# Performance work log

Measured on AMD Instinct MI355X. Metric: run time of the kernel, lower is better.

The kernel has to match this reference:

```python
import jax, jax.numpy as jnp
import numpy as np

B, C, T, E = 8, 64, 128, 256
TYPE_NUM, NF = 40, 128
KS = (5, 4, 3)
NEG = -1e10


def setup_inputs() -> dict:
    key = jax.random.key(0)
    ks = jax.random.split(key, 10)
    s = 0.02
    return {
        "query": jax.random.normal(ks[0], (C, E), jnp.float32),
        "context": jax.random.normal(ks[1], (B, T, E), jnp.float32),
        "mask": jax.random.randint(ks[2], (B, T), 0, 2, jnp.int32),
        "W_hidden": jax.random.normal(ks[3], (4 * E, 4 * E), jnp.float32) * s,
        "b_hidden": jnp.zeros((4 * E,), jnp.float32),
        "W_v": jax.random.normal(ks[4], (1, 4 * E), jnp.float32) * s,
        "b_v": jnp.zeros((1,), jnp.float32),
        "W_lin": jax.random.normal(ks[5], (E, 4 * E), jnp.float32) * s,
        "b_lin": jnp.zeros((E,), jnp.float32),
        "conv_w0": jax.random.normal(ks[6], (NF, E, KS[0]), jnp.float32) * s,
        "conv_b0": jnp.zeros((NF,), jnp.float32),
        "conv_w1": jax.random.normal(ks[7], (NF, E, KS[1]), jnp.float32) * s,
        "conv_b1": jnp.zeros((NF,), jnp.float32),
        "conv_w2": jax.random.normal(ks[8], (NF, E, KS[2]), jnp.float32) * s,
        "conv_b2": jnp.zeros((NF,), jnp.float32),
        "W_cnn": jax.random.normal(ks[9], (TYPE_NUM, NF * 3), jnp.float32) * s,
        "b_cnn": jnp.zeros((TYPE_NUM,), jnp.float32),
    }


def _pair_feat(a, b):
    # [.., e] x2 -> [.., 4e]: [a, b, |a-b|, a*b]
    return jnp.concatenate([a, b, jnp.abs(a - b), a * b], axis=-1)


def _conv1d(x, w, b):
    # x: [b, e, c], w: [f, e, k] (torch Conv1d layout) -> [b, f, c-k+1]
    y = jax.lax.conv_general_dilated(
        x, w, window_strides=(1,), padding="VALID",
        dimension_numbers=("NCH", "OIH", "NCH"))
    return y + b[None, :, None]


def reference(query, context, mask, W_hidden, b_hidden, W_v, b_v,
              W_lin, b_lin, conv_w0, conv_b0, conv_w1, conv_b1,
              conv_w2, conv_b2, W_cnn, b_cnn):
    b, t, e = context.shape
    c = query.shape[0]
    q_ = jnp.broadcast_to(query[None, :, None, :], (b, c, t, e))
    ctx_ = jnp.broadcast_to(context[:, None, :, :], (b, c, t, e))
    feat = _pair_feat(q_, ctx_)                                 # [b,c,t,4e]
    h = jnp.tanh(feat @ W_hidden.T + b_hidden)                  # [b,c,t,4e]
    scores = (h @ W_v.T + b_v)[..., 0]                          # [b,c,t]
    scores = jnp.where((mask < 1)[:, None, :], NEG, scores)
    attn = jax.nn.softmax(scores, axis=-1)                      # [b,c,t]
    g = jnp.einsum("bct,bte->bce", attn, context)               # [b,c,e]
    q2 = jnp.broadcast_to(query[None], (b, c, e))
    h2 = jnp.tanh(_pair_feat(q2, g) @ W_hidden.T + b_hidden)    # [b,c,4e]
    x = h2 @ W_lin.T + b_lin                                    # [b,c,e]
    xT = jnp.transpose(x, (0, 2, 1))                            # [b,e,c]
    pooled = []
    for w, bb in ((conv_w0, conv_b0), (conv_w1, conv_b1), (conv_w2, conv_b2)):
        y = jax.nn.relu(_conv1d(xT, w, bb))                     # [b,f,c-k+1]
        pooled.append(jnp.max(y, axis=2))                       # [b,f]
    cnn = jnp.concatenate(pooled, axis=1)                       # [b,3f]
    return cnn @ W_cnn.T + b_cnn                                # [b,type_num]
```

## Files before the change

kernel.cpp:

```cpp
#include <hip/hip_runtime.h>
#include <math.h>


typedef __bf16 bf16x8 __attribute__((ext_vector_type(8)));
typedef float  f32x4  __attribute__((ext_vector_type(4)));

__device__ __forceinline__ float ftanh(float v) {
    float t = __expf(2.f * v);
    return 1.f - 2.f * __builtin_amdgcn_rcpf(t + 1.f);
}

__device__ __forceinline__ void gld_lds16(const __bf16* g, __bf16* l) {
    __builtin_amdgcn_global_load_lds(
        (const __attribute__((address_space(1))) void*)g,
        (__attribute__((address_space(3))) void*)l, 16, 0, 0);
}

__global__ __launch_bounds__(256) void gemm_tn_kernel(
    const float* __restrict__ A, int lda,
    const float* __restrict__ B, int ldb,
    const float* __restrict__ bias,
    float* __restrict__ C, int ldc, int K)
{
    __shared__ float As[16][68];
    __shared__ float Bs[16][68];
    const int tid = threadIdx.x;
    const int m0 = blockIdx.y * 64, n0 = blockIdx.x * 64;
    const int tm = tid >> 4, tn = tid & 15;
    const int lr = tid >> 2;
    const int lc = (tid & 3) * 4;

    float acc[4][4];
#pragma unroll
    for (int i = 0; i < 4; ++i)
#pragma unroll
        for (int j = 0; j < 4; ++j) acc[i][j] = 0.f;

    for (int k0 = 0; k0 < K; k0 += 16) {
        float4 av = *reinterpret_cast<const float4*>(A + (size_t)(m0 + lr) * lda + k0 + lc);
        float4 bv = *reinterpret_cast<const float4*>(B + (size_t)(n0 + lr) * ldb + k0 + lc);
        As[lc + 0][lr] = av.x; As[lc + 1][lr] = av.y; As[lc + 2][lr] = av.z; As[lc + 3][lr] = av.w;
        Bs[lc + 0][lr] = bv.x; Bs[lc + 1][lr] = bv.y; Bs[lc + 2][lr] = bv.z; Bs[lc + 3][lr] = bv.w;
        __syncthreads();
#pragma unroll
        for (int kk = 0; kk < 16; ++kk) {
            float4 a = *reinterpret_cast<const float4*>(&As[kk][tm * 4]);
            float4 b = *reinterpret_cast<const float4*>(&Bs[kk][tn * 4]);
            float ar[4] = {a.x, a.y, a.z, a.w};
            float br[4] = {b.x, b.y, b.z, b.w};
#pragma unroll
            for (int i = 0; i < 4; ++i)
#pragma unroll
                for (int j = 0; j < 4; ++j) acc[i][j] += ar[i] * br[j];
        }
        __syncthreads();
    }

#pragma unroll
    for (int i = 0; i < 4; ++i) {
        int m = m0 + tm * 4 + i;
        float vals[4];
#pragma unroll
        for (int j = 0; j < 4; ++j) {
            int n = n0 + tn * 4 + j;
            vals[j] = acc[i][j] + (bias ? bias[n] : 0.f);
        }
        float4 o; o.x = vals[0]; o.y = vals[1]; o.z = vals[2]; o.w = vals[3];
        *reinterpret_cast<float4*>(C + (size_t)m * ldc + n0 + tn * 4) = o;
    }
}

__global__ void cvt_kernel(const float* __restrict__ Wh, const float* __restrict__ Wl,
                           const float* __restrict__ ctx,
                           const float* __restrict__ cw0, const float* __restrict__ cw1,
                           const float* __restrict__ cw2,
                           __bf16* __restrict__ Whbf, __bf16* __restrict__ Whbf_t,
                           __bf16* __restrict__ Wlbf, __bf16* __restrict__ ctxbf,
                           float* __restrict__ wt0, float* __restrict__ wt1,
                           float* __restrict__ wt2, float* __restrict__ gsc,
                           float* __restrict__ cnn)
{
    int idx = blockIdx.x * 256 + threadIdx.x;
    if (idx < 131072) {
        const float* s = Wh + (size_t)idx * 8;
        float4 f0 = *reinterpret_cast<const float4*>(s);
        float4 f1 = *reinterpret_cast<const float4*>(s + 4);
        bf16x8 u;
        u[0] = (__bf16)f0.x; u[1] = (__bf16)f0.y; u[2] = (__bf16)f0.z; u[3] = (__bf16)f0.w;
        u[4] = (__bf16)f1.x; u[5] = (__bf16)f1.y; u[6] = (__bf16)f1.z; u[7] = (__bf16)f1.w;
        *reinterpret_cast<bf16x8*>(Whbf + (size_t)idx * 8) = u;
        return;
    }
    if (idx < 196608) {
        int di = idx - 131072;
        int ng = di >> 13, kc = (di >> 10) & 7;
        int row = (di >> 3) & 127, kgp = di & 7;
        int kg = kgp ^ (row & 7);
        const float* s = Wh + (size_t)(ng * 128 + row) * 1024 + 512 + kc * 64 + kg * 8;
        float4 f0 = *reinterpret_cast<const float4*>(s);
        float4 f1 = *reinterpret_cast<const float4*>(s + 4);
        bf16x8 u;
        u[0] = (__bf16)f0.x; u[1] = (__bf16)f0.y; u[2] = (__bf16)f0.z; u[3] = (__bf16)f0.w;
        u[4] = (__bf16)f1.x; u[5] = (__bf16)f1.y; u[6] = (__bf16)f1.z; u[7] = (__bf16)f1.w;
        *reinterpret_cast<bf16x8*>(Whbf_t + (size_t)di * 8) = u;
        return;
    }
    if (idx < 229376) {
        int di = idx - 196608;
        const float* s = Wl + (size_t)di * 8;
        float4 f0 = *reinterpret_cast<const float4*>(s);
        float4 f1 = *reinterpret_cast<const float4*>(s + 4);
        bf16x8 u;
        u[0] = (__bf16)f0.x; u[1] = (__bf16)f0.y; u[2] = (__bf16)f0.z; u[3] = (__bf16)f0.w;
        u[4] = (__bf16)f1.x; u[5] = (__bf16)f1.y; u[6] = (__bf16)f1.z; u[7] = (__bf16)f1.w;
        *reinterpret_cast<bf16x8*>(Wlbf + (size_t)di * 8) = u;
        return;
    }
    if (idx < 262144) {
        int di = idx - 229376;
        const float* s = ctx + (size_t)di * 8;
        float4 f0 = *reinterpret_cast<const float4*>(s);
        float4 f1 = *reinterpret_cast<const float4*>(s + 4);
        bf16x8 u;
        u[0] = (__bf16)f0.x; u[1] = (__bf16)f0.y; u[2] = (__bf16)f0.z; u[3] = (__bf16)f0.w;
        u[4] = (__bf16)f1.x; u[5] = (__bf16)f1.y; u[6] = (__bf16)f1.z; u[7] = (__bf16)f1.w;
        *reinterpret_cast<bf16x8*>(ctxbf + (size_t)di * 8) = u;
        return;
    }
    if (idx < 425984) {
        int j = idx - 262144; int f = j & 127, rest = j >> 7;
        int i = rest % 5, e = rest / 5;
        wt0[j] = cw0[(size_t)(f * 256 + e) * 5 + i]; return;
    }
    if (idx < 557056) {
        int j = idx - 425984; int f = j & 127, rest = j >> 7;
        int i = rest & 3, e = rest >> 2;
        wt1[j] = cw1[(size_t)(f * 256 + e) * 4 + i]; return;
    }
    if (idx < 655360) {
        int j = idx - 557056; int f = j & 127, rest = j >> 7;
        int i = rest % 3, e = rest / 3;
        wt2[j] = cw2[(size_t)(f * 256 + e) * 3 + i]; return;
    }
    if (idx < 671744) {
        int di = idx - 655360;
        reinterpret_cast<float4*>(gsc)[di] = (float4){0.f, 0.f, 0.f, 0.f};
        return;
    }
    if (idx < 674816) cnn[idx - 671744] = 0.f;
}

__global__ __launch_bounds__(512, 4) void attn_mfma_kernel(
    const float* __restrict__ q,
    const float* __restrict__ ctx,
    const __bf16* __restrict__ Whbf_t,
    const float* __restrict__ Wv,
    const float* __restrict__ Apre,
    const float* __restrict__ Bpre,
    float* __restrict__ gsc)
{
    __shared__ __bf16 Us[256 * 64];
    __shared__ __bf16 Ws[128 * 64];
    __shared__ float qc[512];
    __shared__ float sc[256];

    const int tid = threadIdx.x;
    const int cpair = blockIdx.x >> 3, ng = blockIdx.x & 7;
    const int b = cpair >> 5, c0 = (cpair & 31) * 2;
    const int wave = tid >> 6, lane = tid & 63;
    const int w1 = wave & 1, w0 = wave >> 1;
    const int m0 = w0 * 64;
    const int l15 = lane & 15, quad = lane >> 4;
    const int swz = l15 & 7;
    const int kg = tid & 7;

    qc[tid] = q[(size_t)(c0 + (tid >> 8)) * 256 + (tid & 255)];
    if (tid < 256) sc[tid] = 0.f;
    __syncthreads();

    f32x4 acc[4][4];
#pragma unroll
    for (int mi = 0; mi < 4; ++mi)
#pragma unroll
        for (int ni = 0; ni < 4; ++ni) acc[mi][ni] = (f32x4){0.f, 0.f, 0.f, 0.f};

    for (int kc = 0; kc < 8; ++kc) {
        const bool isabs = (kc < 4);
        const int e0 = (kc & 3) * 64;
        const int eb = e0 + kg * 8;
        float qA[8], qB[8];
#pragma unroll
        for (int i = 0; i < 8; ++i) { qA[i] = qc[eb + i]; qB[i] = qc[256 + eb + i]; }
        bf16x8 u0[2], u1[2];
#pragma unroll
        for (int it = 0; it < 2; ++it) {
            const int trow = it * 64 + (tid >> 3);
            const float* cp = ctx + (size_t)(b * 128 + trow) * 256 + eb;
            float4 cl0 = *reinterpret_cast<const float4*>(cp);
            float4 cl1 = *reinterpret_cast<const float4*>(cp + 4);
            float cv[8] = {cl0.x, cl0.y, cl0.z, cl0.w, cl1.x, cl1.y, cl1.z, cl1.w};
#pragma unroll
            for (int i = 0; i < 8; ++i) {
                u0[it][i] = (__bf16)(isabs ? fabsf(qA[i] - cv[i]) : qA[i] * cv[i]);
                u1[it][i] = (__bf16)(isabs ? fabsf(qB[i] - cv[i]) : qB[i] * cv[i]);
            }
        }
        __syncthreads();
        const __bf16* wtile = Whbf_t + (size_t)(ng * 8 + kc) * 8192;
#pragma unroll
        for (int it = 0; it < 2; ++it) {
            int gidx = wave * 128 + it * 64;
            gld_lds16(wtile + (size_t)(gidx + lane) * 8, &Ws[gidx * 8]);
        }
#pragma unroll
        for (int it = 0; it < 2; ++it) {
            const int trow = it * 64 + (tid >> 3);
            const int off = (kg ^ (trow & 7)) * 8;
            *reinterpret_cast<bf16x8*>(&Us[trow * 64 + off]) = u0[it];
            *reinterpret_cast<bf16x8*>(&Us[(trow + 128) * 64 + off]) = u1[it];
        }
        __syncthreads();
#pragma unroll
        for (int ks = 0; ks < 2; ++ks) {
            const int c8 = (((ks * 4 + quad) ^ swz)) * 8;
            bf16x8 a[4], bfr[4];
#pragma unroll
            for (int mi = 0; mi < 4; ++mi)
                a[mi] = *reinterpret_cast<const bf16x8*>(
                    &Us[(m0 + mi * 16 + l15) * 64 + c8]);
#pragma unroll
            for (int ni = 0; ni < 4; ++ni)
                bfr[ni] = *reinterpret_cast<const bf16x8*>(
                    &Ws[(w1 * 64 + ni * 16 + l15) * 64 + c8]);
#pragma unroll
            for (int mi = 0; mi < 4; ++mi)
#pragma unroll
                for (int ni = 0; ni < 4; ++ni)
                    acc[mi][ni] = __builtin_amdgcn_mfma_f32_16x16x32_bf16(
                        a[mi], bfr[ni], acc[mi][ni], 0, 0, 0);
        }
    }

    const int jcol = ng * 128 + w1 * 64 + l15;
    const int c = c0 + (w0 >> 1);
    float av[4], wv[4];
#pragma unroll
    for (int ni = 0; ni < 4; ++ni) {
        av[ni] = Apre[(size_t)c * 1024 + jcol + ni * 16];
        wv[ni] = Wv[jcol + ni * 16];
    }
#pragma unroll
    for (int mi = 0; mi < 4; ++mi) {
        const int tb = (w0 & 1) * 64 + mi * 16 + quad * 4;
        float p[4];
#pragma unroll
        for (int r = 0; r < 4; ++r) {
            const float* bp = Bpre + (size_t)(b * 128 + tb + r) * 1024 + jcol;
            float s = 0.f;
#pragma unroll
            for (int ni = 0; ni < 4; ++ni)
                s += ftanh(acc[mi][ni][r] + av[ni] + bp[ni * 16]) * wv[ni];
            p[r] = s;
        }
#pragma unroll
        for (int off = 1; off < 16; off <<= 1)
#pragma unroll
            for (int r = 0; r < 4; ++r) p[r] += __shfl_xor(p[r], off, 16);
        if (l15 == 0) {
#pragma unroll
            for (int r = 0; r < 4; ++r)
                atomicAdd(&sc[(w0 >> 1) * 128 + tb + r], p[r]);
        }
    }
    __syncthreads();

    if (tid < 256) atomicAdd(&gsc[(size_t)(b * 64 + c0) * 128 + tid], sc[tid]);
}

__global__ __launch_bounds__(256) void attn_tail_kernel(
    const float* __restrict__ ctx, const int* __restrict__ mask,
    const float* __restrict__ bv, const float* __restrict__ gsc,
    const float* __restrict__ q, __bf16* __restrict__ feat2)
{
    __shared__ float sc[128];
    __shared__ float red;
    const int tid = threadIdx.x;
    const int bc = blockIdx.x, b = bc >> 6, c = bc & 63;

    if (tid < 128) {
        float s = gsc[(size_t)bc * 128 + tid] + bv[0];
        if (mask[b * 128 + tid] < 1) s = -1e10f;
        sc[tid] = s;
    }
    __syncthreads();
    if (tid < 64) {
        float m = fmaxf(sc[tid], sc[tid + 64]);
        for (int off = 32; off; off >>= 1) m = fmaxf(m, __shfl_xor(m, off, 64));
        if (tid == 0) red = m;
    }
    __syncthreads();
    const float mx = red;
    if (tid < 128) sc[tid] = __expf(sc[tid] - mx);
    __syncthreads();
    if (tid < 64) {
        float s = sc[tid] + sc[tid + 64];
        for (int off = 32; off; off >>= 1) s += __shfl_xor(s, off, 64);
        if (tid == 0) red = s;
    }
    __syncthreads();
    const float inv = 1.f / red;

    float gv = 0.f;
    for (int t = 0; t < 128; ++t) gv += sc[t] * ctx[(size_t)(b * 128 + t) * 256 + tid];
    gv *= inv;
    const float qv = q[(size_t)c * 256 + tid];
    __bf16* o = feat2 + (size_t)bc * 768 + tid;
    o[0]   = (__bf16)gv;
    o[256] = (__bf16)fabsf(qv - gv);
    o[512] = (__bf16)(qv * gv);
}

template <int ACT, int OUTBF, int BMODE>
__global__ __launch_bounds__(256) void mfma_gemm_kernel(
    const __bf16* __restrict__ A, int lda,
    const __bf16* __restrict__ B, int ldb,
    const float* __restrict__ bias, void* __restrict__ Cout,
    int K, int ldc)
{
    __shared__ __bf16 As[64 * 72];
    __shared__ __bf16 Bs[64 * 72];
    const int tid = threadIdx.x;
    const int wave = tid >> 6, lane = tid & 63;
    const int w0 = wave >> 1, w1 = wave & 1;
    const int l15 = lane & 15, quad = lane >> 4;
    const int m0 = blockIdx.y * 64, n0 = blockIdx.x * 64;

    f32x4 acc[2][2];
#pragma unroll
    for (int mi = 0; mi < 2; ++mi)
#pragma unroll
        for (int ni = 0; ni < 2; ++ni) acc[mi][ni] = (f32x4){0.f, 0.f, 0.f, 0.f};

    for (int k0 = 0; k0 < K; k0 += 64) {
        __syncthreads();
#pragma unroll
        for (int it = 0; it < 2; ++it) {
            int idx = tid + it * 256;
            int row = idx >> 3, kgi = idx & 7;
            int4 va = *reinterpret_cast<const int4*>(A + (size_t)(m0 + row) * lda + k0 + kgi * 8);
            *reinterpret_cast<int4*>(&As[row * 72 + kgi * 8]) = va;
            int4 vb = *reinterpret_cast<const int4*>(B + (size_t)(n0 + row) * ldb + k0 + kgi * 8);
            *reinterpret_cast<int4*>(&Bs[row * 72 + kgi * 8]) = vb;
        }
        __syncthreads();
#pragma unroll
        for (int ks = 0; ks < 2; ++ks) {
            bf16x8 a[2], bb[2];
#pragma unroll
            for (int mi = 0; mi < 2; ++mi)
                a[mi] = *reinterpret_cast<const bf16x8*>(
                    &As[(w0 * 32 + mi * 16 + l15) * 72 + ks * 32 + quad * 8]);
#pragma unroll
            for (int ni = 0; ni < 2; ++ni)
                bb[ni] = *reinterpret_cast<const bf16x8*>(
                    &Bs[(w1 * 32 + ni * 16 + l15) * 72 + ks * 32 + quad * 8]);
#pragma unroll
            for (int mi = 0; mi < 2; ++mi)
#pragma unroll
                for (int ni = 0; ni < 2; ++ni)
                    acc[mi][ni] = __builtin_amdgcn_mfma_f32_16x16x32_bf16(
                        a[mi], bb[ni], acc[mi][ni], 0, 0, 0);
        }
    }

#pragma unroll
    for (int mi = 0; mi < 2; ++mi)
#pragma unroll
        for (int ni = 0; ni < 2; ++ni) {
            int col = n0 + w1 * 32 + ni * 16 + l15;
#pragma unroll
            for (int r = 0; r < 4; ++r) {
                int row = m0 + w0 * 32 + mi * 16 + quad * 4 + r;
                float bsv = (BMODE == 0) ? bias[col]
                          : (BMODE == 1) ? bias[(row & 63) * 1024 + col] : 0.f;
                float v = acc[mi][ni][r] + bsv;
                if (ACT) v = ftanh(v);
                if (OUTBF) ((__bf16*)Cout)[(size_t)row * ldc + col] = (__bf16)v;
                else       ((float*)Cout)[(size_t)row * ldc + col] = v;
            }
        }
}

template <int KW>
__device__ __forceinline__ void conv_body(
    const float* __restrict__ x, const float* __restrict__ wt,
    float* __restrict__ part, int b, int chunk, int bi_part, int pbase, float* xs)
{
    const int tid = threadIdx.x;
    const int f = tid & 127, esub = tid >> 7;
    const int e0 = chunk * 64;

#pragma unroll
    for (int it = 0; it < 16; ++it) {
        int idx = tid + it * 256;
        int e = idx & 63, p = idx >> 6;
        xs[e * 72 + p] = x[(size_t)(b * 64 + p) * 256 + e0 + e];
    }
    __syncthreads();

    float acc[32];
#pragma unroll
    for (int p = 0; p < 32; ++p) acc[p] = 0.f;

    for (int ei = 0; ei < 32; ++ei) {
        const int eL = esub * 32 + ei;
        float wreg[KW];
#pragma unroll
        for (int i = 0; i < KW; ++i)
            wreg[i] = wt[(size_t)((e0 + eL) * KW + i) * 128 + f];
        float xv[36];
#pragma unroll
        for (int k4 = 0; k4 < 9; ++k4) {
            float4 v = *reinterpret_cast<const float4*>(&xs[eL * 72 + pbase + k4 * 4]);
            xv[k4 * 4 + 0] = v.x; xv[k4 * 4 + 1] = v.y;
            xv[k4 * 4 + 2] = v.z; xv[k4 * 4 + 3] = v.w;
        }
#pragma unroll
        for (int i = 0; i < KW; ++i)
#pragma unroll
            for (int p = 0; p < 32; ++p)
                acc[p] = fmaf(wreg[i], xv[p + i], acc[p]);
    }

    float* op = part + ((size_t)(bi_part * 2 + esub)) * 8192 + f;
#pragma unroll
    for (int p = 0; p < 32; ++p) op[(pbase + p) * 128] = acc[p];
}

__global__ __launch_bounds__(256) void conv_partial_kernel(
    const float* __restrict__ x,
    const float* __restrict__ wt0, const float* __restrict__ wt1,
    const float* __restrict__ wt2, float* __restrict__ part)
{
    __shared__ float xs[64 * 72];
    const int bi = blockIdx.x;
    const int kw = bi >> 6, b = (bi >> 3) & 7, chunk = (bi >> 1) & 3;
    const int pbase = (bi & 1) * 32;
    const int bi_part = kw * 32 + b * 4 + chunk;
    if (kw == 0)      conv_body<5>(x, wt0, part, b, chunk, bi_part, pbase, xs);
    else if (kw == 1) conv_body<4>(x, wt1, part, b, chunk, bi_part, pbase, xs);
    else              conv_body<3>(x, wt2, part, b, chunk, bi_part, pbase, xs);
}

__global__ __launch_bounds__(128) void reduce_pool_kernel(
    const float* __restrict__ part,
    const float* __restrict__ b0, const float* __restrict__ b1,
    const float* __restrict__ b2, float* __restrict__ cnn)
{
    const int bi = blockIdx.x;
    const int kw = bi >> 6, b = (bi >> 3) & 7, pc = bi & 7;
    const int f = threadIdx.x;
    const int KW = 5 - kw, P = 64 - KW + 1;
    const float bias = (kw == 0 ? b0 : kw == 1 ? b1 : b2)[f];
    float mx = 0.f;
#pragma unroll
    for (int pl = 0; pl < 8; ++pl) {
        int p = pc * 8 + pl;
        if (p < P) {
            float s = 0.f;
#pragma unroll
            for (int c4 = 0; c4 < 4; ++c4)
#pragma unroll
                for (int es = 0; es < 2; ++es)
                    s += part[((size_t)((kw * 32 + b * 4 + c4) * 2 + es)) * 8192 + p * 128 + f];
            s += bias;
            mx = fmaxf(mx, s);
        }
    }
    if (mx > 0.f)
        atomicMax((int*)(cnn + b * 384 + kw * 128 + f), __float_as_int(mx));
}

__global__ void final_kernel(const float* __restrict__ cnn, const float* __restrict__ Wc,
                             const float* __restrict__ bc, float* __restrict__ out)
{
    int o = threadIdx.x;
    if (o >= 320) return;
    int b = o / 40, t = o - b * 40;
    float s = bc[t];
    for (int i = 0; i < 384; ++i) s += cnn[b * 384 + i] * Wc[t * 384 + i];
    out[o] = s;
}

extern "C" void kernel_launch(void* const* d_in, const int* in_sizes, int n_in,
                              void* d_out, int out_size, void* d_ws, size_t ws_size,
                              hipStream_t stream)
{
    (void)in_sizes; (void)n_in; (void)out_size; (void)ws_size;
    const float* q    = (const float*)d_in[0];
    const float* ctx  = (const float*)d_in[1];
    const int*   mask = (const int*)d_in[2];
    const float* Wh   = (const float*)d_in[3];
    const float* bh   = (const float*)d_in[4];
    const float* Wv   = (const float*)d_in[5];
    const float* bv   = (const float*)d_in[6];
    const float* Wl   = (const float*)d_in[7];
    const float* bl   = (const float*)d_in[8];
    const float* cw0  = (const float*)d_in[9];
    const float* cb0  = (const float*)d_in[10];
    const float* cw1  = (const float*)d_in[11];
    const float* cb1  = (const float*)d_in[12];
    const float* cw2  = (const float*)d_in[13];
    const float* cb2  = (const float*)d_in[14];
    const float* Wc   = (const float*)d_in[15];
    const float* bc   = (const float*)d_in[16];

    float* ws   = (float*)d_ws;
    float* Apre = ws;
    float* g    = Apre + 65536;
    float* x    = g + 131072;
    float* cnn  = x + 131072;
    float* part = cnn + 3072;
    float* wt0  = part + 1572864;
    float* wt1  = wt0 + 163840;
    float* wt2  = wt1 + 131072;
    __bf16* bfb    = (__bf16*)(wt2 + 98304);
    __bf16* Whbf   = bfb;
    __bf16* Wlbf   = bfb + 1048576;
    __bf16* feat2b = bfb + 1310720;
    __bf16* h2b    = bfb + 1703936;
    float*  gsc    = (float*)(bfb + 2228224);
    __bf16* Whbf_t = (__bf16*)part;
    __bf16* ctxbf  = Whbf_t + 524288;
    float*  Bpre   = (float*)(ctxbf + 262144);

    dim3 blk(256);
    cvt_kernel<<<2636, blk, 0, stream>>>(Wh, Wl, ctx, cw0, cw1, cw2,
                                         Whbf, Whbf_t, Wlbf, ctxbf, wt0, wt1, wt2,
                                         gsc, cnn);
    gemm_tn_kernel<<<dim3(16, 1), blk, 0, stream>>>(q, 256, Wh, 1024, bh, Apre, 1024, 256);
    mfma_gemm_kernel<0, 0, 2><<<dim3(16, 16), blk, 0, stream>>>(
        ctxbf, 256, Whbf + 256, 1024, nullptr, Bpre, 256, 1024);
    attn_mfma_kernel<<<2048, dim3(512), 0, stream>>>(q, ctx, Whbf_t, Wv, Apre, Bpre, gsc);
    attn_tail_kernel<<<512, blk, 0, stream>>>(ctx, mask, bv, gsc, q, feat2b);
    mfma_gemm_kernel<1, 1, 1><<<dim3(16, 8), blk, 0, stream>>>(
        feat2b, 768, Whbf + 256, 1024, Apre, h2b, 768, 1024);
    mfma_gemm_kernel<0, 0, 0><<<dim3(4, 8), blk, 0, stream>>>(
        h2b, 1024, Wlbf, 1024, bl, x, 1024, 256);
    conv_partial_kernel<<<192, blk, 0, stream>>>(x, wt0, wt1, wt2, part);
    reduce_pool_kernel<<<192, dim3(128), 0, stream>>>(part, cb0, cb1, cb2, cnn);
    final_kernel<<<1, 320, 0, stream>>>(cnn, Wc, bc, (float*)d_out);
}
```

Before: 299.9 us.

## Fuse query precompute GEMM into convert kernel and split-K the W_lin GEMM

```diff
diff --git a/kernel.cpp b/kernel.cpp
--- a/kernel.cpp
+++ b/kernel.cpp
@@ -16,71 +16,67 @@
         (__attribute__((address_space(3))) void*)l, 16, 0, 0);
 }
 
-__global__ __launch_bounds__(256) void gemm_tn_kernel(
-    const float* __restrict__ A, int lda,
-    const float* __restrict__ B, int ldb,
-    const float* __restrict__ bias,
-    float* __restrict__ C, int ldc, int K)
-{
-    __shared__ float As[16][68];
-    __shared__ float Bs[16][68];
-    const int tid = threadIdx.x;
-    const int m0 = blockIdx.y * 64, n0 = blockIdx.x * 64;
-    const int tm = tid >> 4, tn = tid & 15;
-    const int lr = tid >> 2;
-    const int lc = (tid & 3) * 4;
-
-    float acc[4][4];
-#pragma unroll
-    for (int i = 0; i < 4; ++i)
-#pragma unroll
-        for (int j = 0; j < 4; ++j) acc[i][j] = 0.f;
-
-    for (int k0 = 0; k0 < K; k0 += 16) {
-        float4 av = *reinterpret_cast<const float4*>(A + (size_t)(m0 + lr) * lda + k0 + lc);
-        float4 bv = *reinterpret_cast<const float4*>(B + (size_t)(n0 + lr) * ldb + k0 + lc);
-        As[lc + 0][lr] = av.x; As[lc + 1][lr] = av.y; As[lc + 2][lr] = av.z; As[lc + 3][lr] = av.w;
-        Bs[lc + 0][lr] = bv.x; Bs[lc + 1][lr] = bv.y; Bs[lc + 2][lr] = bv.z; Bs[lc + 3][lr] = bv.w;
-        __syncthreads();
-#pragma unroll
-        for (int kk = 0; kk < 16; ++kk) {
-            float4 a = *reinterpret_cast<const float4*>(&As[kk][tm * 4]);
-            float4 b = *reinterpret_cast<const float4*>(&Bs[kk][tn * 4]);
-            float ar[4] = {a.x, a.y, a.z, a.w};
-            float br[4] = {b.x, b.y, b.z, b.w};
-#pragma unroll
-            for (int i = 0; i < 4; ++i)
-#pragma unroll
-                for (int j = 0; j < 4; ++j) acc[i][j] += ar[i] * br[j];
-        }
-        __syncthreads();
-    }
-
-#pragma unroll
-    for (int i = 0; i < 4; ++i) {
-        int m = m0 + tm * 4 + i;
-        float vals[4];
-#pragma unroll
-        for (int j = 0; j < 4; ++j) {
-            int n = n0 + tn * 4 + j;
-            vals[j] = acc[i][j] + (bias ? bias[n] : 0.f);
-        }
-        float4 o; o.x = vals[0]; o.y = vals[1]; o.z = vals[2]; o.w = vals[3];
-        *reinterpret_cast<float4*>(C + (size_t)m * ldc + n0 + tn * 4) = o;
-    }
-}
-
-__global__ void cvt_kernel(const float* __restrict__ Wh, const float* __restrict__ Wl,
-                           const float* __restrict__ ctx,
-                           const float* __restrict__ cw0, const float* __restrict__ cw1,
-                           const float* __restrict__ cw2,
-                           __bf16* __restrict__ Whbf, __bf16* __restrict__ Whbf_t,
-                           __bf16* __restrict__ Wlbf, __bf16* __restrict__ ctxbf,
-                           float* __restrict__ wt0, float* __restrict__ wt1,
-                           float* __restrict__ wt2, float* __restrict__ gsc,
-                           float* __restrict__ cnn)
-{
-    int idx = blockIdx.x * 256 + threadIdx.x;
+__global__ __launch_bounds__(256) void cvt_kernel(
+    const float* __restrict__ Wh, const float* __restrict__ Wl,
+    const float* __restrict__ ctx,
+    const float* __restrict__ cw0, const float* __restrict__ cw1,
+    const float* __restrict__ cw2,
+    const float* __restrict__ q, const float* __restrict__ bh,
+    float* __restrict__ Apre, float* __restrict__ x,
+    __bf16* __restrict__ Whbf, __bf16* __restrict__ Whbf_t,
+    __bf16* __restrict__ Wlbf, __bf16* __restrict__ ctxbf,
+    float* __restrict__ wt0, float* __restrict__ wt1,
+    float* __restrict__ wt2, float* __restrict__ gsc,
+    float* __restrict__ cnn)
+{
+    if (blockIdx.x < 16) {
+        __shared__ float As[16][68];
+        __shared__ float Bs[16][68];
+        const int tid = threadIdx.x;
+        const int n0 = blockIdx.x * 64;
+        const int tm = tid >> 4, tn = tid & 15;
+        const int lr = tid >> 2;
+        const int lc = (tid & 3) * 4;
+
+        float acc[4][4];
+#pragma unroll
+        for (int i = 0; i < 4; ++i)
+#pragma unroll
+            for (int j = 0; j < 4; ++j) acc[i][j] = 0.f;
+
+        for (int k0 = 0; k0 < 256; k0 += 16) {
+            float4 av = *reinterpret_cast<const float4*>(q + (size_t)lr * 256 + k0 + lc);
+            float4 bv = *reinterpret_cast<const float4*>(Wh + (size_t)(n0 + lr) * 1024 + k0 + lc);
+            As[lc + 0][lr] = av.x; As[lc + 1][lr] = av.y; As[lc + 2][lr] = av.z; As[lc + 3][lr] = av.w;
+            Bs[lc + 0][lr] = bv.x; Bs[lc + 1][lr] = bv.y; Bs[lc + 2][lr] = bv.z; Bs[lc + 3][lr] = bv.w;
+            __syncthreads();
+#pragma unroll
+            for (int kk = 0; kk < 16; ++kk) {
+                float4 a = *reinterpret_cast<const float4*>(&As[kk][tm * 4]);
+                float4 b = *reinterpret_cast<const float4*>(&Bs[kk][tn * 4]);
+                float ar[4] = {a.x, a.y, a.z, a.w};
+                float br[4] = {b.x, b.y, b.z, b.w};
+#pragma unroll
+                for (int i = 0; i < 4; ++i)
+#pragma unroll
+                    for (int j = 0; j < 4; ++j) acc[i][j] += ar[i] * br[j];
+            }
+            __syncthreads();
+        }
+
+#pragma unroll
+        for (int i = 0; i < 4; ++i) {
+            int m = tm * 4 + i;
+            float vals[4];
+#pragma unroll
+            for (int j = 0; j < 4; ++j) vals[j] = acc[i][j] + bh[n0 + tn * 4 + j];
+            float4 o; o.x = vals[0]; o.y = vals[1]; o.z = vals[2]; o.w = vals[3];
+            *reinterpret_cast<float4*>(Apre + (size_t)m * 1024 + n0 + tn * 4) = o;
+        }
+        return;
+    }
+
+    int idx = (blockIdx.x - 16) * 256 + threadIdx.x;
     if (idx < 131072) {
         const float* s = Wh + (size_t)idx * 8;
         float4 f0 = *reinterpret_cast<const float4*>(s);
@@ -147,7 +143,11 @@
         reinterpret_cast<float4*>(gsc)[di] = (float4){0.f, 0.f, 0.f, 0.f};
         return;
     }
-    if (idx < 674816) cnn[idx - 671744] = 0.f;
+    if (idx < 674816) { cnn[idx - 671744] = 0.f; return; }
+    if (idx < 707584) {
+        int di = idx - 674816;
+        reinterpret_cast<float4*>(x)[di] = (float4){0.f, 0.f, 0.f, 0.f};
+    }
 }
 
 __global__ __launch_bounds__(512, 4) void attn_mfma_kernel(
@@ -320,7 +320,7 @@
     o[512] = (__bf16)(qv * gv);
 }
 
-template <int ACT, int OUTBF, int BMODE>
+template <int ACT, int OUTBF, int BMODE, int ATOMIC>
 __global__ __launch_bounds__(256) void mfma_gemm_kernel(
     const __bf16* __restrict__ A, int lda,
     const __bf16* __restrict__ B, int ldb,
@@ -335,13 +335,20 @@
     const int l15 = lane & 15, quad = lane >> 4;
     const int m0 = blockIdx.y * 64, n0 = blockIdx.x * 64;
 
+    int kbeg = 0, kend = K;
+    if (ATOMIC) {
+        int kchunk = K / gridDim.z;
+        kbeg = blockIdx.z * kchunk;
+        kend = kbeg + kchunk;
+    }
+
     f32x4 acc[2][2];
 #pragma unroll
     for (int mi = 0; mi < 2; ++mi)
 #pragma unroll
         for (int ni = 0; ni < 2; ++ni) acc[mi][ni] = (f32x4){0.f, 0.f, 0.f, 0.f};
 
-    for (int k0 = 0; k0 < K; k0 += 64) {
+    for (int k0 = kbeg; k0 < kend; k0 += 64) {
         __syncthreads();
 #pragma unroll
         for (int it = 0; it < 2; ++it) {
@@ -383,10 +390,15 @@
                 int row = m0 + w0 * 32 + mi * 16 + quad * 4 + r;
                 float bsv = (BMODE == 0) ? bias[col]
                           : (BMODE == 1) ? bias[(row & 63) * 1024 + col] : 0.f;
-                float v = acc[mi][ni][r] + bsv;
-                if (ACT) v = ftanh(v);
-                if (OUTBF) ((__bf16*)Cout)[(size_t)row * ldc + col] = (__bf16)v;
-                else       ((float*)Cout)[(size_t)row * ldc + col] = v;
+                if (ATOMIC) {
+                    float v = acc[mi][ni][r] + (blockIdx.z == 0 ? bsv : 0.f);
+                    atomicAdd((float*)Cout + (size_t)row * ldc + col, v);
+                } else {
+                    float v = acc[mi][ni][r] + bsv;
+                    if (ACT) v = ftanh(v);
+                    if (OUTBF) ((__bf16*)Cout)[(size_t)row * ldc + col] = (__bf16)v;
+                    else       ((float*)Cout)[(size_t)row * ldc + col] = v;
+                }
             }
         }
 }
@@ -535,17 +547,16 @@
     float*  Bpre   = (float*)(ctxbf + 262144);
 
     dim3 blk(256);
-    cvt_kernel<<<2636, blk, 0, stream>>>(Wh, Wl, ctx, cw0, cw1, cw2,
+    cvt_kernel<<<2780, blk, 0, stream>>>(Wh, Wl, ctx, cw0, cw1, cw2, q, bh, Apre, x,
                                          Whbf, Whbf_t, Wlbf, ctxbf, wt0, wt1, wt2,
                                          gsc, cnn);
-    gemm_tn_kernel<<<dim3(16, 1), blk, 0, stream>>>(q, 256, Wh, 1024, bh, Apre, 1024, 256);
-    mfma_gemm_kernel<0, 0, 2><<<dim3(16, 16), blk, 0, stream>>>(
+    mfma_gemm_kernel<0, 0, 2, 0><<<dim3(16, 16), blk, 0, stream>>>(
         ctxbf, 256, Whbf + 256, 1024, nullptr, Bpre, 256, 1024);
     attn_mfma_kernel<<<2048, dim3(512), 0, stream>>>(q, ctx, Whbf_t, Wv, Apre, Bpre, gsc);
     attn_tail_kernel<<<512, blk, 0, stream>>>(ctx, mask, bv, gsc, q, feat2b);
-    mfma_gemm_kernel<1, 1, 1><<<dim3(16, 8), blk, 0, stream>>>(
+    mfma_gemm_kernel<1, 1, 1, 0><<<dim3(16, 8), blk, 0, stream>>>(
         feat2b, 768, Whbf + 256, 1024, Apre, h2b, 768, 1024);
-    mfma_gemm_kernel<0, 0, 0><<<dim3(4, 8), blk, 0, stream>>>(
+    mfma_gemm_kernel<0, 0, 0, 1><<<dim3(4, 8, 4), blk, 0, stream>>>(
         h2b, 1024, Wlbf, 1024, bl, x, 1024, 256);
     conv_partial_kernel<<<192, blk, 0, stream>>>(x, wt0, wt1, wt2, part);
     reduce_pool_kernel<<<192, dim3(128), 0, stream>>>(part, cb0, cb1, cb2, cnn);
```

After: 279.2 us. 1.07x faster.
